# Kernel tuning notes

Measured on AMD Instinct MI355X. Metric: run time of the kernel, lower is better.

The kernel has to match this reference:

```python
import jax, jax.numpy as jnp
import numpy as np

NH0 = 8          # per-head channels (min(max(512//64,2),8))
NHEADS = 4       # assumed einpool head count == number of equivariant eqs
NSTACKS = 4      # max(min(8//2,4),1)
MARGIN = 8.0
F = NH0 * NHEADS  # 32


def _mlp2(x, w1, b1, w2, b2):
    # 2-layer MLP: Linear -> ReLU -> Linear (matches MLP with nlayers=2)
    return jnp.maximum(x @ w1 + b1, 0.0) @ w2 + b2


def _mixed_pool(h, mask):
    # h: (B,C,A,W,F), mask: (B,C,A,W,1)
    B, C, A, W, Fc = h.shape
    # sin-transformed multi-head equivariant einsum pool over axes (a,b)
    y = jnp.sin(h).reshape(B, C, A, W, NH0, NHEADS) * mask[..., None]
    e0 = y[..., 0]                                                        # identity head
    e1 = jnp.broadcast_to(jnp.sum(y[..., 1], axis=3, keepdims=True), e0.shape)  # sum over b
    e2 = jnp.broadcast_to(jnp.sum(y[..., 2], axis=2, keepdims=True), e0.shape)  # sum over a
    e3 = jnp.broadcast_to(jnp.sum(y[..., 3], axis=(2, 3), keepdims=True), e0.shape)  # sum over a,b
    h0 = jnp.concatenate([e0, e1, e2, e3], axis=-1)                       # (B,C,A,W,NH0*4)
    # cascaded 4-way max pool over b, a, C (equivalent to joint max), broadcast back
    h1 = jnp.broadcast_to(jnp.max(h, axis=(1, 2, 3), keepdims=True), h.shape)
    return jnp.concatenate([h0, h1], axis=-1)                             # (B,C,A,W,2F)


def setup_inputs() -> dict:
    key = jax.random.key(0)
    ks = jax.random.split(key, 16)
    B, C, A, W = 8, 24, 96, 96
    nh = 128
    x = jax.random.normal(ks[0], (B, C, A, W), jnp.float32)
    rows_len = jax.random.randint(ks[1], (B, C), 48, A + 1, jnp.int32)
    cols_len = jax.random.randint(ks[2], (B, C), 48, W + 1, jnp.int32)

    def lin(k, fi, fo):
        return jax.random.normal(k, (fi, fo), jnp.float32) / np.float32(np.sqrt(fi))

    inp = {
        'x': x, 'rows_len': rows_len, 'cols_len': cols_len,
        't0_w1': lin(ks[3], 1, nh), 't0_b1': jnp.zeros((nh,), jnp.float32),
        't0_w2': lin(ks[4], nh, F), 't0_b2': jnp.zeros((F,), jnp.float32),
        't_w1': jax.random.normal(ks[5], (NSTACKS, 2 * F, nh), jnp.float32) / np.float32(np.sqrt(2 * F)),
        't_b1': jnp.zeros((NSTACKS, nh), jnp.float32),
        't_w2': jax.random.normal(ks[6], (NSTACKS, nh, F), jnp.float32) / np.float32(np.sqrt(nh)),
        't_b2': jnp.zeros((NSTACKS, F), jnp.float32),
        'tout_w1': lin(ks[7], F, nh), 'tout_b1': jnp.zeros((nh,), jnp.float32),
        'tout_w2': lin(ks[8], nh, 2), 'tout_b2': jnp.zeros((2,), jnp.float32),
    }
    return inp


def reference(x, rows_len, cols_len, t0_w1, t0_b1, t0_w2, t0_b2,
              t_w1, t_b1, t_w2, t_b2, tout_w1, tout_b1, tout_w2, tout_b2):
    B, C, A, W = x.shape
    # ragged validity mask from per-matrix (rows, cols) lengths (nested-tensor pad)
    ra = jnp.arange(A, dtype=jnp.int32)
    rb = jnp.arange(W, dtype=jnp.int32)
    m = ((ra[:, None] < rows_len[..., None, None]) &
         (rb[None, :] < cols_len[..., None, None])).astype(x.dtype)      # (B,C,A,W)
    # per-matrix normalization over valid region (torch .std is unbiased)
    n = jnp.sum(m, axis=(-1, -2), keepdims=True)
    mean = jnp.sum(x * m, axis=(-1, -2), keepdims=True) / jnp.maximum(n, 1.0)
    var = jnp.sum(((x - mean) ** 2) * m, axis=(-1, -2), keepdims=True) / jnp.maximum(n - 1.0, 1.0)
    std = jnp.maximum(jnp.sqrt(var), 1e-12)
    h = (((x - mean) / std) * m)[..., None]                               # (B,C,A,W,1)
    mask = m[..., None]                                                   # (B,C,A,W,1)

    h = _mlp2(h, t0_w1, t0_b1, t0_w2, t0_b2)                              # (B,C,A,W,F)
    for i in range(NSTACKS):
        h = h * mask
        skip = h
        hp = _mixed_pool(h, mask)
        h = skip + _mlp2(hp, t_w1[i], t_b1[i], t_w2[i], t_b2[i])
        h = h * mask

    num = jnp.clip(jnp.sum(h * h, axis=(2, 3)), 1e-20, None)              # (B,C,F)
    den = jnp.clip(jnp.sum(mask, axis=(2, 3)), 1e-12, None)               # (B,C,1)
    h = jnp.sqrt(num / den)
    h = jnp.mean(h, axis=1)                                               # (B,F)
    out = MARGIN * jnp.tanh(_mlp2(h, tout_w1, tout_b1, tout_w2, tout_b2))  # (B,2)
    return out
```

## Files before the change

### kernel.cpp

```cpp
#include <hip/hip_runtime.h>
#include <math.h>
#include <float.h>

#define NB 8
#define NC 24
#define NA 96
#define NW 96
#define NF 32
#define NHID 128
#define AW (NA*NW)
#define NBC (NB*NC)
#define NEL ((size_t)NBC*AW)
#define HSTR 17

typedef float v2f __attribute__((ext_vector_type(2)));
typedef float f32x4 __attribute__((ext_vector_type(4)));
typedef short short8_t __attribute__((ext_vector_type(8)));
#ifndef __has_builtin
#define __has_builtin(x) 0
#endif
#if __has_builtin(__builtin_elementwise_fma)
#define PKFMA(a,b,c) __builtin_elementwise_fma((a),(b),(c))
#else
#define PKFMA(a,b,c) ((a)*(b)+(c))
#endif

union frag_u { unsigned int u[4]; short8_t s; };

__device__ __forceinline__ unsigned short bf16rne(float x) {
    unsigned int u = __float_as_uint(x);
    unsigned int r = u + 0x7fffu + ((u >> 16) & 1u);
    return (unsigned short)(r >> 16);
}
__device__ __forceinline__ unsigned fkey(float x) {
    unsigned u = __float_as_uint(x);
    return (u >> 31) ? ~u : (u | 0x80000000u);
}
__device__ __forceinline__ float funkey(unsigned k) {
    return (k >> 31) ? __uint_as_float(k ^ 0x80000000u) : __uint_as_float(~k);
}

__global__ __launch_bounds__(256) void stats_kernel(
    const float* __restrict__ x, const int* __restrict__ rows_len,
    const int* __restrict__ cols_len, float* __restrict__ stats)
{
    int bc = blockIdx.x;
    int R = rows_len[bc], L = cols_len[bc];
    const float* xp = x + (size_t)bc * AW;
    int n = R * L;
    float sx = 0.f, sxx = 0.f;
    for (int i = threadIdx.x; i < n; i += 256) {
        int a = i / L, w = i - a * L;
        float v = xp[a * NW + w];
        sx += v;
        sxx = fmaf(v, v, sxx);
    }
    __shared__ float r1[256], r2[256];
    r1[threadIdx.x] = sx; r2[threadIdx.x] = sxx;
    __syncthreads();
    for (int s = 128; s > 0; s >>= 1) {
        if (threadIdx.x < s) {
            r1[threadIdx.x] += r1[threadIdx.x + s];
            r2[threadIdx.x] += r2[threadIdx.x + s];
        }
        __syncthreads();
    }
    if (threadIdx.x == 0) {
        float fn = (float)n;
        float mean = r1[0] / fn;
        float var = fmaxf((r2[0] - r1[0] * r1[0] / fn) / (fn - 1.f), 0.f);
        float sd = fmaxf(sqrtf(var), 1e-12f);
        stats[2 * bc] = mean;
        stats[2 * bc + 1] = 1.f / sd;
    }
}

__global__ __launch_bounds__(256) void prep_kernel(
    const float* __restrict__ tw1, float* __restrict__ w1t)
{
    int i = blockIdx.x * 256 + threadIdx.x;
    if (i >= 4 * NHID * 24) return;
    int s = i / (NHID * 24), r = i % (NHID * 24);
    int j = r / 24, t = r % 24;
    w1t[i] = tw1[(size_t)s * 64 * NHID + t * NHID + j];
}

__global__ __launch_bounds__(256) void prep2_kernel(
    const float* __restrict__ tw2, unsigned short* __restrict__ w2bf)
{
    int i = blockIdx.x * 256 + threadIdx.x;
    if (i >= 4 * NF * NHID) return;
    int s = i / (NF * NHID), r = i % (NF * NHID);
    int f = r / NHID, j = r % NHID;
    float v = tw2[((size_t)s * NHID + j) * NF + f];
    unsigned short hi = bf16rne(v);
    float hf = __uint_as_float(((unsigned int)hi) << 16);
    unsigned short lo = bf16rne(v - hf);
    size_t base = (size_t)s * (2 * NF * NHID) + (size_t)f * NHID + j;
    w2bf[base] = hi;
    w2bf[base + NF * NHID] = lo;
}

__global__ __launch_bounds__(256) void t0_kernel(
    const float* __restrict__ x, const int* __restrict__ rows_len,
    const int* __restrict__ cols_len, const float* __restrict__ stats,
    const float* __restrict__ w1, const float* __restrict__ b1,
    const float* __restrict__ w2, const float* __restrict__ b2,
    float* __restrict__ h)
{
    int tid = threadIdx.x;
    int bc = blockIdx.x / 18;
    int base = (blockIdx.x % 18) * 512;
    int R = rows_len[bc], L = cols_len[bc];
    float mean = stats[2 * bc], rstd = stats[2 * bc + 1];

    int eA = base + tid, eB = eA + 256;
    int aA = eA / NW, wA = eA % NW;
    int aB = eB / NW, wB = eB % NW;
    bool vA = (aA < R) && (wA < L);
    bool vB = (aB < R) && (wB < L);
    size_t gA = (size_t)bc * AW + eA;
    float xA = vA ? (x[gA] - mean) * rstd : 0.f;
    float xB = vB ? (x[gA + 256] - mean) * rstd : 0.f;

    v2f oA[16], oB[16];
    const v2f* b22 = (const v2f*)b2;
    #pragma unroll
    for (int i = 0; i < 16; i++) { v2f bb = b22[i]; oA[i] = bb; oB[i] = bb; }
    for (int j = 0; j < NHID; j++) {
        float hA = fmaxf(fmaf(xA, w1[j], b1[j]), 0.f);
        float hB = fmaxf(fmaf(xB, w1[j], b1[j]), 0.f);
        const v2f* wr = (const v2f*)&w2[j * NF];
        v2f hA2 = {hA, hA}, hB2 = {hB, hB};
        #pragma unroll
        for (int i = 0; i < 16; i++) {
            v2f q = wr[i];
            oA[i] = PKFMA(hA2, q, oA[i]);
            oB[i] = PKFMA(hB2, q, oB[i]);
        }
    }
    float mA = vA ? 1.f : 0.f, mB = vB ? 1.f : 0.f;
    float* hp = h + (size_t)bc * NF * AW;
    #pragma unroll
    for (int f = 0; f < NF; f++) {
        hp[(size_t)f * AW + eA] = oA[f >> 1][f & 1] * mA;
        hp[(size_t)f * AW + eB] = oB[f >> 1][f & 1] * mB;
    }
}

__global__ __launch_bounds__(256) void pool_kernel(
    const float* __restrict__ h, float* __restrict__ rowsum,
    float* __restrict__ colsum, float* __restrict__ matsum,
    unsigned* __restrict__ cmax_key)
{
    __shared__ float sred[4];
    __shared__ float scol[4][96];
    int blk = blockIdx.x;
    int bc = blk >> 5, f = blk & 31;
    const float* p = h + (size_t)blk * AW;
    int tid = threadIdx.x;
    int lane = tid & 63, wv = tid >> 6;

    float mx = -FLT_MAX;
    for (int i = tid; i < AW; i += 256) mx = fmaxf(mx, p[i]);
    #pragma unroll
    for (int off = 32; off >= 1; off >>= 1) mx = fmaxf(mx, __shfl_xor(mx, off, 64));
    if (lane == 0) sred[wv] = mx;
    __syncthreads();
    if (tid == 0)
        cmax_key[bc * NF + f] =
            fkey(fmaxf(fmaxf(sred[0], sred[1]), fmaxf(sred[2], sred[3])));

    int mode = f & 3, k = f >> 2;
    if (mode == 1) {
        for (int r = 0; r < 24; r++) {
            int a = wv + 4 * r;
            float v1 = p[a * NW + lane];
            float s = __sinf(v1);
            if (lane < 32) s += __sinf(p[a * NW + 64 + lane]);
            #pragma unroll
            for (int off = 32; off >= 1; off >>= 1) s += __shfl_xor(s, off, 64);
            if (lane == 0) rowsum[(bc * NA + a) * 8 + k] = s;
        }
    } else if (mode == 2) {
        float acc0 = 0.f, acc1 = 0.f;
        for (int r = 0; r < 24; r++) {
            int a = wv + 4 * r;
            acc0 += __sinf(p[a * NW + lane]);
            if (lane < 32) acc1 += __sinf(p[a * NW + 64 + lane]);
        }
        scol[wv][lane] = acc0;
        if (lane < 32) scol[wv][64 + lane] = acc1;
        __syncthreads();
        if (tid < 96)
            colsum[(bc * NW + tid) * 8 + k] =
                scol[0][tid] + scol[1][tid] + scol[2][tid] + scol[3][tid];
    } else if (mode == 3) {
        float s = 0.f;
        for (int i = tid; i < AW; i += 256) s += __sinf(p[i]);
        #pragma unroll
        for (int off = 32; off >= 1; off >>= 1) s += __shfl_xor(s, off, 64);
        __syncthreads();
        if (lane == 0) sred[wv] = s;
        __syncthreads();
        if (tid == 0) matsum[bc * 8 + k] = sred[0] + sred[1] + sred[2] + sred[3];
    }
}

__global__ __launch_bounds__(256) void precomp_kernel(
    const float* __restrict__ rowsum, const float* __restrict__ colsum,
    const float* __restrict__ matsum, const unsigned* __restrict__ cmax_key,
    const float* __restrict__ w1, const float* __restrict__ b1,
    float* __restrict__ rowc, float* __restrict__ colc)
{
    __shared__ float sbm[NF];
    __shared__ float sconst[NHID];
    __shared__ float scs[NW * 8];
    int tid = threadIdx.x;
    int bc = blockIdx.x, b = bc / NC;

    for (int i = tid; i < NW * 8; i += 256) scs[i] = colsum[bc * NW * 8 + i];
    if (tid < NF) {
        unsigned km = cmax_key[(b * NC) * NF + tid];
        for (int c = 1; c < NC; c++) {
            unsigned kc = cmax_key[(b * NC + c) * NF + tid];
            km = (kc > km) ? kc : km;
        }
        sbm[tid] = funkey(km);
    }
    __syncthreads();
    if (tid < NHID) {
        float v = b1[tid];
        const float* mp = matsum + bc * 8;
        #pragma unroll
        for (int k = 0; k < 8; k++) v = fmaf(mp[k], w1[(24 + k) * NHID + tid], v);
        #pragma unroll
        for (int f = 0; f < NF; f++) v = fmaf(sbm[f], w1[(32 + f) * NHID + tid], v);
        sconst[tid] = v;
    }
    __syncthreads();
    for (int i = tid; i < NHID * NA; i += 256) {
        int j = i / NA, aa = i - j * NA;
        const float* rp = rowsum + (bc * NA + aa) * 8;
        float v = sconst[j];
        #pragma unroll
        for (int k = 0; k < 8; k++) v = fmaf(rp[k], w1[(8 + k) * NHID + j], v);
        rowc[(size_t)bc * (NHID * NA) + i] = v;
    }
    for (int i = tid; i < NHID * NW; i += 256) {
        int j = i / NW, ww = i - j * NW;
        float v = 0.f;
        #pragma unroll
        for (int k = 0; k < 8; k++) v = fmaf(scs[ww * 8 + k], w1[(16 + k) * NHID + j], v);
        colc[(size_t)bc * (NHID * NW) + i] = v;
    }
}

__global__ __launch_bounds__(256, 4) void mlp_kernel(
    float* __restrict__ h, const float* __restrict__ rowc,
    const float* __restrict__ colc, const int* __restrict__ rows_len,
    const int* __restrict__ cols_len, const float* __restrict__ w1t,
    const unsigned short* __restrict__ w2bf, const float* __restrict__ b2,
    float* __restrict__ sqsum, float* __restrict__ rowsum,
    float* __restrict__ colsum, float* __restrict__ matsum,
    unsigned* __restrict__ cmax_key, int last, int do_pool)
{
    __shared__ unsigned int hid_hi[256 * HSTR];
    __shared__ unsigned int hid_lo[256 * HSTR];

    int tid = threadIdx.x;
    int bc = blockIdx.x / 36;
    int blk36 = blockIdx.x % 36;
    int base = blk36 * 256;
    int lane = tid & 63, wv = tid >> 6;
    int g = lane >> 4, c16 = lane & 15;

    int e = base + tid;
    int a = e / NW, wc = e - a * NW;
    float* hp = h + (size_t)bc * NF * AW;

    float p[8];
    #pragma unroll
    for (int k = 0; k < 8; k++) p[k] = __sinf(hp[(size_t)(4 * k) * AW + e]);
    v2f p2[4];
    #pragma unroll
    for (int t = 0; t < 4; t++) p2[t] = (v2f){p[2 * t], p[2 * t + 1]};

    const unsigned short* w2hi = w2bf;
    const unsigned short* w2lo = w2bf + NF * NHID;

    f32x4 acc[4][2];
    #pragma unroll
    for (int t = 0; t < 2; t++) {
        f32x4 bb = *(const f32x4*)(b2 + 16 * t + 4 * g);
        #pragma unroll
        for (int ti = 0; ti < 4; ti++) acc[ti][t] = bb;
    }

    const float* rcr = rowc + (size_t)bc * (NHID * NA);
    const float* rcc = colc + (size_t)bc * (NHID * NW);

    for (int w = 0; w < 4; w++) {
        int jw = 32 * w;
        frag_u Ah[2], Al[2];
        #pragma unroll
        for (int t = 0; t < 2; t++) {
            size_t off = (size_t)(c16 + 16 * t) * NHID + jw + 8 * g;
            const unsigned int* ph = (const unsigned int*)(w2hi + off);
            const unsigned int* pl = (const unsigned int*)(w2lo + off);
            #pragma unroll
            for (int d = 0; d < 4; d++) { Ah[t].u[d] = ph[d]; Al[t].u[d] = pl[d]; }
        }

        #pragma unroll 4
        for (int jp = 0; jp < 16; jp++) {
            int jl = 2 * jp;
            const v2f* w1r0 = (const v2f*)(w1t + (size_t)(jw + jl) * 24);
            const v2f* w1r1 = w1r0 + 12;
            v2f u0 = {rcr[(size_t)(jw + jl) * NA + a], rcc[(size_t)(jw + jl) * NW + wc]};
            v2f u1 = {rcr[(size_t)(jw + jl + 1) * NA + a], rcc[(size_t)(jw + jl + 1) * NW + wc]};
            #pragma unroll
            for (int t = 0; t < 4; t++) {
                u0 = PKFMA(p2[t], w1r0[t], u0);
                u1 = PKFMA(p2[t], w1r1[t], u1);
            }
            float v0 = fmaxf(u0.x + u0.y, 0.f);
            float v1 = fmaxf(u1.x + u1.y, 0.f);
            unsigned int hi, lo;
            asm("v_cvt_pk_bf16_f32 %0, %1, %2" : "=v"(hi) : "v"(v0), "v"(v1));
            float h0 = __uint_as_float(hi << 16);
            float h1 = __uint_as_float(hi & 0xffff0000u);
            float l0 = v0 - h0, l1 = v1 - h1;
            asm("v_cvt_pk_bf16_f32 %0, %1, %2" : "=v"(lo) : "v"(l0), "v"(l1));
            hid_hi[tid * HSTR + jp] = hi;
            hid_lo[tid * HSTR + jp] = lo;
        }
        __syncthreads();

        #pragma unroll
        for (int ti = 0; ti < 4; ti++) {
            int el = (wv * 4 + ti) * 16 + c16;
            const unsigned int* bh = &hid_hi[el * HSTR + 4 * g];
            const unsigned int* bl = &hid_lo[el * HSTR + 4 * g];
            frag_u Bh, Bl;
            #pragma unroll
            for (int d = 0; d < 4; d++) { Bh.u[d] = bh[d]; Bl.u[d] = bl[d]; }
            #pragma unroll
            for (int t = 0; t < 2; t++) {
                acc[ti][t] = __builtin_amdgcn_mfma_f32_16x16x32_bf16(Ah[t].s, Bh.s, acc[ti][t], 0, 0, 0);
                acc[ti][t] = __builtin_amdgcn_mfma_f32_16x16x32_bf16(Al[t].s, Bh.s, acc[ti][t], 0, 0, 0);
                acc[ti][t] = __builtin_amdgcn_mfma_f32_16x16x32_bf16(Ah[t].s, Bl.s, acc[ti][t], 0, 0, 0);
            }
        }
        __syncthreads();
    }

    float* col_lds = (float*)hid_hi;
    float* row_lds = col_lds + 96 * 9;
    float* mat_lds = row_lds + 32;
    unsigned* max_lds = (unsigned*)(mat_lds + 8);
    if (do_pool) {
        for (int i = tid; i < 96 * 9 + 32 + 8 + 32; i += 256) col_lds[i] = 0.f;
        __syncthreads();
    }

    int R = rows_len[bc], L = cols_len[bc];
    int a0 = base / NW;
    float psum[2][4] = {{0.f, 0.f, 0.f, 0.f}, {0.f, 0.f, 0.f, 0.f}};
    float matp[2] = {0.f, 0.f};
    float mxp[2][4];
    #pragma unroll
    for (int t = 0; t < 2; t++)
        #pragma unroll
        for (int r = 0; r < 4; r++) mxp[t][r] = -FLT_MAX;

    #pragma unroll
    for (int ti = 0; ti < 4; ti++) {
        int el = (wv * 4 + ti) * 16 + c16;
        int ee = base + el;
        int aa = ee / NW, ww = ee - aa * NW;
        float mk = (aa < R && ww < L) ? 1.f : 0.f;
        float rowv[2];
        #pragma unroll
        for (int t = 0; t < 2; t++) {
            #pragma unroll
            for (int r = 0; r < 4; r++) {
                int f = 4 * g + r + 16 * t;
                float* ad = hp + (size_t)f * AW + ee;
                float hv = (*ad + acc[ti][t][r]) * mk;
                if (!last) *ad = hv;
                else       psum[t][r] = fmaf(hv, hv, psum[t][r]);
                if (do_pool) {
                    mxp[t][r] = fmaxf(mxp[t][r], hv);
                    if (r == 1)      rowv[t] = __sinf(hv);
                    else if (r == 2) atomicAdd(&col_lds[ww * 9 + g + 4 * t], __sinf(hv));
                    else if (r == 3) matp[t] += __sinf(hv);
                }
            }
        }
        if (do_pool) {
            #pragma unroll
            for (int t = 0; t < 2; t++) {
                float v = rowv[t];
                v += __shfl_xor(v, 1, 64);
                v += __shfl_xor(v, 2, 64);
                v += __shfl_xor(v, 4, 64);
                v += __shfl_xor(v, 8, 64);
                if (c16 == 0) atomicAdd(&row_lds[(aa - a0) * 8 + g + 4 * t], v);
            }
        }
    }

    if (do_pool) {
        #pragma unroll
        for (int t = 0; t < 2; t++) {
            float v = matp[t];
            v += __shfl_xor(v, 1, 64);
            v += __shfl_xor(v, 2, 64);
            v += __shfl_xor(v, 4, 64);
            v += __shfl_xor(v, 8, 64);
            if (c16 == 0) atomicAdd(&mat_lds[g + 4 * t], v);
            #pragma unroll
            for (int r = 0; r < 4; r++) {
                float m = mxp[t][r];
                m = fmaxf(m, __shfl_xor(m, 1, 64));
                m = fmaxf(m, __shfl_xor(m, 2, 64));
                m = fmaxf(m, __shfl_xor(m, 4, 64));
                m = fmaxf(m, __shfl_xor(m, 8, 64));
                if (c16 == 0) atomicMax(&max_lds[4 * g + r + 16 * t], fkey(m));
            }
        }
        __syncthreads();
        if (tid < 32) {
            int ar = a0 + (tid >> 3);
            if (ar < NA) atomicAdd(&rowsum[(bc * NA + ar) * 8 + (tid & 7)], row_lds[tid]);
        }
        if (tid < 8) atomicAdd(&matsum[bc * 8 + tid], mat_lds[tid]);
        if (tid >= 32 && tid < 64) atomicMax(&cmax_key[bc * NF + tid - 32], max_lds[tid - 32]);
        for (int i = tid; i < NW * 8; i += 256)
            atomicAdd(&colsum[bc * NW * 8 + i], col_lds[(i >> 3) * 9 + (i & 7)]);
    }

    if (last) {
        float* sq_lds = (float*)hid_hi;
        if (tid < NF) sq_lds[tid] = 0.f;
        __syncthreads();
        #pragma unroll
        for (int t = 0; t < 2; t++) {
            #pragma unroll
            for (int r = 0; r < 4; r++) {
                float v = psum[t][r];
                v += __shfl_xor(v, 1, 64);
                v += __shfl_xor(v, 2, 64);
                v += __shfl_xor(v, 4, 64);
                v += __shfl_xor(v, 8, 64);
                if (c16 == 0) atomicAdd(&sq_lds[4 * g + r + 16 * t], v);
            }
        }
        __syncthreads();
        if (tid < NF) atomicAdd(&sqsum[bc * NF + tid], sq_lds[tid]);
    }
}

__global__ __launch_bounds__(64) void out_kernel(
    const float* __restrict__ sqsum, const int* __restrict__ rows_len,
    const int* __restrict__ cols_len, const float* __restrict__ w1,
    const float* __restrict__ b1, const float* __restrict__ w2,
    const float* __restrict__ b2, float* __restrict__ out)
{
    int b = threadIdx.x;
    if (b >= NB) return;
    float hm[NF];
    #pragma unroll
    for (int f = 0; f < NF; f++) hm[f] = 0.f;
    for (int c = 0; c < NC; c++) {
        int bc = b * NC + c;
        float n = (float)(rows_len[bc] * cols_len[bc]);
        float rdn = 1.f / fmaxf(n, 1e-12f);
        #pragma unroll
        for (int f = 0; f < NF; f++) {
            float q = fmaxf(sqsum[bc * NF + f], 1e-20f);
            hm[f] += sqrtf(q * rdn);
        }
    }
    #pragma unroll
    for (int f = 0; f < NF; f++) hm[f] *= (1.f / (float)NC);

    float o0 = b2[0], o1 = b2[1];
    for (int j = 0; j < NHID; j++) {
        float v = b1[j];
        #pragma unroll
        for (int f = 0; f < NF; f++) v = fmaf(hm[f], w1[f * NHID + j], v);
        v = fmaxf(v, 0.f);
        o0 = fmaf(v, w2[j * 2 + 0], o0);
        o1 = fmaf(v, w2[j * 2 + 1], o1);
    }
    out[b * 2 + 0] = 8.f * tanhf(o0);
    out[b * 2 + 1] = 8.f * tanhf(o1);
}

extern "C" void kernel_launch(void* const* d_in, const int* in_sizes, int n_in,
                              void* d_out, int out_size, void* d_ws, size_t ws_size,
                              hipStream_t stream)
{
    const float* x    = (const float*)d_in[0];
    const int* rl     = (const int*)d_in[1];
    const int* cl     = (const int*)d_in[2];
    const float* t0w1 = (const float*)d_in[3];
    const float* t0b1 = (const float*)d_in[4];
    const float* t0w2 = (const float*)d_in[5];
    const float* t0b2 = (const float*)d_in[6];
    const float* tw1  = (const float*)d_in[7];
    const float* tb1  = (const float*)d_in[8];
    const float* tw2  = (const float*)d_in[9];
    const float* tb2  = (const float*)d_in[10];
    const float* ow1  = (const float*)d_in[11];
    const float* ob1  = (const float*)d_in[12];
    const float* ow2  = (const float*)d_in[13];
    const float* ob2  = (const float*)d_in[14];
    float* out = (float*)d_out;

    float* ws    = (float*)d_ws;
    float* h     = ws;
    float* stats = h + NEL * NF;
    float*    rowb = stats + 2 * NBC;
    float*    matb = rowb + (size_t)NBC * NA * 8;
    unsigned* cmxb = (unsigned*)(matb + NBC * 8);
    float*    colb = (float*)(cmxb + NBC * NF);
    size_t    accum_floats = (size_t)NBC * NA * 8 + NBC * 8 + NBC * NF
                           + (size_t)NBC * NW * 8;
    float* sqb   = colb + (size_t)NBC * NW * 8;
    float* w1tb  = sqb + NBC * NF;
    float* rowcb = w1tb + 4 * NHID * 24;
    float* colcb = rowcb + (size_t)NBC * NHID * NA;
    unsigned short* w2bfb = (unsigned short*)(colcb + (size_t)NBC * NHID * NW);

    hipMemsetAsync(sqb, 0, NBC * NF * sizeof(float), stream);
    stats_kernel<<<NBC, 256, 0, stream>>>(x, rl, cl, stats);
    prep_kernel<<<(4 * NHID * 24 + 255) / 256, 256, 0, stream>>>(tw1, w1tb);
    prep2_kernel<<<(4 * NF * NHID + 255) / 256, 256, 0, stream>>>(tw2, w2bfb);
    t0_kernel<<<(int)(NEL / 512), 256, 0, stream>>>(x, rl, cl, stats,
                                                    t0w1, t0b1, t0w2, t0b2, h);
    pool_kernel<<<NBC * NF, 256, 0, stream>>>(h, rowb, colb, matb, cmxb);
    for (int s = 0; s < 4; s++) {
        precomp_kernel<<<NBC, 256, 0, stream>>>(rowb, colb, matb, cmxb,
            tw1 + (size_t)s * 64 * NHID, tb1 + s * NHID, rowcb, colcb);
        if (s < 3)
            hipMemsetAsync(rowb, 0, accum_floats * sizeof(float), stream);
        mlp_kernel<<<NBC * 36, 256, 0, stream>>>(h, rowcb, colcb, rl, cl,
            w1tb + (size_t)s * NHID * 24,
            w2bfb + (size_t)s * (2 * NF * NHID),
            tb2 + s * NF, sqb, rowb, colb, matb, cmxb,
            (s == 3) ? 1 : 0, (s < 3) ? 1 : 0);
    }
    out_kernel<<<1, 64, 0, stream>>>(sqb, rl, cl, ow1, ob1, ow2, ob2, out);
}
```

Before: 1.383 ms.

## Fuse initial pooling reductions into t0 kernel and drop separate pool pass

The t0 MLP kernel now computes the row, column and matrix sin-sums and the per-channel max directly from its register outputs. It reduces them through shared-memory atomics and then global atomics, which removes the separate pool_kernel that re-read the full h tensor. Element-to-thread mapping is changed so each 16-lane group covers contiguous elements of one row for the group reductions. It also adds an upfront memset of the accumulators, more global atomics, extra LDS, and a launch bound of 4 blocks per SM that may constrain registers.

Result: no change. 1.366 ms (-1.2%).

```diff
diff --git a/kernel.cpp b/kernel.cpp
--- a/kernel.cpp
+++ b/kernel.cpp
@@ -39,6 +39,20 @@
 __device__ __forceinline__ float funkey(unsigned k) {
     return (k >> 31) ? __uint_as_float(k ^ 0x80000000u) : __uint_as_float(~k);
 }
+__device__ __forceinline__ float grp16_sum(float v) {
+    v += __shfl_xor(v, 1, 64);
+    v += __shfl_xor(v, 2, 64);
+    v += __shfl_xor(v, 4, 64);
+    v += __shfl_xor(v, 8, 64);
+    return v;
+}
+__device__ __forceinline__ float grp16_max(float v) {
+    v = fmaxf(v, __shfl_xor(v, 1, 64));
+    v = fmaxf(v, __shfl_xor(v, 2, 64));
+    v = fmaxf(v, __shfl_xor(v, 4, 64));
+    v = fmaxf(v, __shfl_xor(v, 8, 64));
+    return v;
+}
 
 __global__ __launch_bounds__(256) void stats_kernel(
     const float* __restrict__ x, const int* __restrict__ rows_len,
@@ -101,27 +115,42 @@
     w2bf[base + NF * NHID] = lo;
 }
 
-__global__ __launch_bounds__(256) void t0_kernel(
+__global__ __launch_bounds__(256, 4) void t0_kernel(
     const float* __restrict__ x, const int* __restrict__ rows_len,
     const int* __restrict__ cols_len, const float* __restrict__ stats,
     const float* __restrict__ w1, const float* __restrict__ b1,
     const float* __restrict__ w2, const float* __restrict__ b2,
-    float* __restrict__ h)
-{
+    float* __restrict__ h, float* __restrict__ rowsum,
+    float* __restrict__ colsum, float* __restrict__ matsum,
+    unsigned* __restrict__ cmax_key)
+{
+    __shared__ float col_lds[96 * 9];
+    __shared__ float row_lds[8 * 8];
+    __shared__ float mat_lds[8];
+    __shared__ unsigned max_lds[NF];
+
     int tid = threadIdx.x;
     int bc = blockIdx.x / 18;
     int base = (blockIdx.x % 18) * 512;
+    int lane = tid & 63, wv = tid >> 6;
+    int c16 = lane & 15;
     int R = rows_len[bc], L = cols_len[bc];
     float mean = stats[2 * bc], rstd = stats[2 * bc + 1];
 
-    int eA = base + tid, eB = eA + 256;
+    for (int i = tid; i < 96 * 9; i += 256) col_lds[i] = 0.f;
+    if (tid < 64) row_lds[tid] = 0.f;
+    if (tid < 8) mat_lds[tid] = 0.f;
+    if (tid < NF) max_lds[tid] = 0u;
+
+    int eA = base + wv * 128 + lane;
+    int eB = eA + 64;
     int aA = eA / NW, wA = eA % NW;
     int aB = eB / NW, wB = eB % NW;
     bool vA = (aA < R) && (wA < L);
     bool vB = (aB < R) && (wB < L);
     size_t gA = (size_t)bc * AW + eA;
     float xA = vA ? (x[gA] - mean) * rstd : 0.f;
-    float xB = vB ? (x[gA + 256] - mean) * rstd : 0.f;
+    float xB = vB ? (x[gA + 64] - mean) * rstd : 0.f;
 
     v2f oA[16], oB[16];
     const v2f* b22 = (const v2f*)b2;
@@ -146,65 +175,49 @@
         hp[(size_t)f * AW + eA] = oA[f >> 1][f & 1] * mA;
         hp[(size_t)f * AW + eB] = oB[f >> 1][f & 1] * mB;
     }
-}
-
-__global__ __launch_bounds__(256) void pool_kernel(
-    const float* __restrict__ h, float* __restrict__ rowsum,
-    float* __restrict__ colsum, float* __restrict__ matsum,
-    unsigned* __restrict__ cmax_key)
-{
-    __shared__ float sred[4];
-    __shared__ float scol[4][96];
-    int blk = blockIdx.x;
-    int bc = blk >> 5, f = blk & 31;
-    const float* p = h + (size_t)blk * AW;
-    int tid = threadIdx.x;
-    int lane = tid & 63, wv = tid >> 6;
-
-    float mx = -FLT_MAX;
-    for (int i = tid; i < AW; i += 256) mx = fmaxf(mx, p[i]);
-    #pragma unroll
-    for (int off = 32; off >= 1; off >>= 1) mx = fmaxf(mx, __shfl_xor(mx, off, 64));
-    if (lane == 0) sred[wv] = mx;
     __syncthreads();
-    if (tid == 0)
-        cmax_key[bc * NF + f] =
-            fkey(fmaxf(fmaxf(sred[0], sred[1]), fmaxf(sred[2], sred[3])));
-
-    int mode = f & 3, k = f >> 2;
-    if (mode == 1) {
-        for (int r = 0; r < 24; r++) {
-            int a = wv + 4 * r;
-            float v1 = p[a * NW + lane];
-            float s = __sinf(v1);
-            if (lane < 32) s += __sinf(p[a * NW + 64 + lane]);
-            #pragma unroll
-            for (int off = 32; off >= 1; off >>= 1) s += __shfl_xor(s, off, 64);
-            if (lane == 0) rowsum[(bc * NA + a) * 8 + k] = s;
-        }
-    } else if (mode == 2) {
-        float acc0 = 0.f, acc1 = 0.f;
-        for (int r = 0; r < 24; r++) {
-            int a = wv + 4 * r;
-            acc0 += __sinf(p[a * NW + lane]);
-            if (lane < 32) acc1 += __sinf(p[a * NW + 64 + lane]);
-        }
-        scol[wv][lane] = acc0;
-        if (lane < 32) scol[wv][64 + lane] = acc1;
-        __syncthreads();
-        if (tid < 96)
-            colsum[(bc * NW + tid) * 8 + k] =
-                scol[0][tid] + scol[1][tid] + scol[2][tid] + scol[3][tid];
-    } else if (mode == 3) {
-        float s = 0.f;
-        for (int i = tid; i < AW; i += 256) s += __sinf(p[i]);
-        #pragma unroll
-        for (int off = 32; off >= 1; off >>= 1) s += __shfl_xor(s, off, 64);
-        __syncthreads();
-        if (lane == 0) sred[wv] = s;
-        __syncthreads();
-        if (tid == 0) matsum[bc * 8 + k] = sred[0] + sred[1] + sred[2] + sred[3];
-    }
+
+    int a0 = base / NW;
+    int rowA = aA - a0, rowB = aB - a0;
+    float matp[8];
+    #pragma unroll
+    for (int k = 0; k < 8; k++) matp[k] = 0.f;
+
+    #pragma unroll
+    for (int k = 0; k < 8; k++) {
+        int fr = 4 * k + 1;
+        float sA = grp16_sum(__sinf(oA[fr >> 1][fr & 1] * mA));
+        float sB = grp16_sum(__sinf(oB[fr >> 1][fr & 1] * mB));
+        if (c16 == 0) {
+            atomicAdd(&row_lds[rowA * 8 + k], sA);
+            atomicAdd(&row_lds[rowB * 8 + k], sB);
+        }
+        int fc = 4 * k + 2;
+        atomicAdd(&col_lds[wA * 9 + k], __sinf(oA[fc >> 1][fc & 1] * mA));
+        atomicAdd(&col_lds[wB * 9 + k], __sinf(oB[fc >> 1][fc & 1] * mB));
+        int fm = 4 * k + 3;
+        matp[k] = __sinf(oA[fm >> 1][fm & 1] * mA) + __sinf(oB[fm >> 1][fm & 1] * mB);
+    }
+    #pragma unroll
+    for (int k = 0; k < 8; k++) {
+        float v = grp16_sum(matp[k]);
+        if (c16 == 0) atomicAdd(&mat_lds[k], v);
+    }
+    #pragma unroll
+    for (int f = 0; f < NF; f++) {
+        float v = grp16_max(fmaxf(oA[f >> 1][f & 1] * mA, oB[f >> 1][f & 1] * mB));
+        if (c16 == 0) atomicMax(&max_lds[f], fkey(v));
+    }
+    __syncthreads();
+
+    if (tid < 48) {
+        int ar = a0 + (tid >> 3);
+        if (ar < NA) atomicAdd(&rowsum[(bc * NA + ar) * 8 + (tid & 7)], row_lds[tid]);
+    }
+    if (tid < 8) atomicAdd(&matsum[bc * 8 + tid], mat_lds[tid]);
+    if (tid >= 32 && tid < 64) atomicMax(&cmax_key[bc * NF + tid - 32], max_lds[tid - 32]);
+    for (int i = tid; i < NW * 8; i += 256)
+        atomicAdd(&colsum[bc * NW * 8 + i], col_lds[(i >> 3) * 9 + (i & 7)]);
 }
 
 __global__ __launch_bounds__(256) void precomp_kernel(
@@ -401,11 +414,7 @@
         if (do_pool) {
             #pragma unroll
             for (int t = 0; t < 2; t++) {
-                float v = rowv[t];
-                v += __shfl_xor(v, 1, 64);
-                v += __shfl_xor(v, 2, 64);
-                v += __shfl_xor(v, 4, 64);
-                v += __shfl_xor(v, 8, 64);
+                float v = grp16_sum(rowv[t]);
                 if (c16 == 0) atomicAdd(&row_lds[(aa - a0) * 8 + g + 4 * t], v);
             }
         }
@@ -414,19 +423,11 @@
     if (do_pool) {
         #pragma unroll
         for (int t = 0; t < 2; t++) {
-            float v = matp[t];
-            v += __shfl_xor(v, 1, 64);
-            v += __shfl_xor(v, 2, 64);
-            v += __shfl_xor(v, 4, 64);
-            v += __shfl_xor(v, 8, 64);
+            float v = grp16_sum(matp[t]);
             if (c16 == 0) atomicAdd(&mat_lds[g + 4 * t], v);
             #pragma unroll
             for (int r = 0; r < 4; r++) {
-                float m = mxp[t][r];
-                m = fmaxf(m, __shfl_xor(m, 1, 64));
-                m = fmaxf(m, __shfl_xor(m, 2, 64));
-                m = fmaxf(m, __shfl_xor(m, 4, 64));
-                m = fmaxf(m, __shfl_xor(m, 8, 64));
+                float m = grp16_max(mxp[t][r]);
                 if (c16 == 0) atomicMax(&max_lds[4 * g + r + 16 * t], fkey(m));
             }
         }
@@ -449,11 +450,7 @@
         for (int t = 0; t < 2; t++) {
             #pragma unroll
             for (int r = 0; r < 4; r++) {
-                float v = psum[t][r];
-                v += __shfl_xor(v, 1, 64);
-                v += __shfl_xor(v, 2, 64);
-                v += __shfl_xor(v, 4, 64);
-                v += __shfl_xor(v, 8, 64);
+                float v = grp16_sum(psum[t][r]);
                 if (c16 == 0) atomicAdd(&sq_lds[4 * g + r + 16 * t], v);
             }
         }
@@ -536,12 +533,13 @@
     unsigned short* w2bfb = (unsigned short*)(colcb + (size_t)NBC * NHID * NW);
 
     hipMemsetAsync(sqb, 0, NBC * NF * sizeof(float), stream);
+    hipMemsetAsync(rowb, 0, accum_floats * sizeof(float), stream);
     stats_kernel<<<NBC, 256, 0, stream>>>(x, rl, cl, stats);
     prep_kernel<<<(4 * NHID * 24 + 255) / 256, 256, 0, stream>>>(tw1, w1tb);
     prep2_kernel<<<(4 * NF * NHID + 255) / 256, 256, 0, stream>>>(tw2, w2bfb);
     t0_kernel<<<(int)(NEL / 512), 256, 0, stream>>>(x, rl, cl, stats,
-                                                    t0w1, t0b1, t0w2, t0b2, h);
-    pool_kernel<<<NBC * NF, 256, 0, stream>>>(h, rowb, colb, matb, cmxb);
+                                                    t0w1, t0b1, t0w2, t0b2, h,
+                                                    rowb, colb, matb, cmxb);
     for (int s = 0; s < 4; s++) {
         precomp_kernel<<<NBC, 256, 0, stream>>>(rowb, colb, matb, cmxb,
             tw1 + (size_t)s * 64 * NHID, tb1 + s * NHID, rowcb, colcb);
```
